# Kernel tuning notes

Hardware: AMD Instinct MI355X
Metric: run time of the kernel (lower is better)

Reference implementation:

```python
import jax, jax.numpy as jnp
import numpy as np

N_NODES = 50000
N_EDGES = 800000
N_GRAPHS = 64

def _glorot(key, shape, scale=0.05):
    return jax.random.normal(key, shape, dtype=jnp.float32) * scale

def setup_inputs() -> dict:
    key = jax.random.key(0)
    ks = jax.random.split(key, 32)
    inp = {
        'x': jax.random.normal(ks[0], (N_NODES, 17), dtype=jnp.float32),
        'edge_index': jax.random.randint(ks[1], (2, N_EDGES), 0, N_NODES, dtype=jnp.int64) if jax.config.jax_enable_x64 else jax.random.randint(ks[1], (2, N_EDGES), 0, N_NODES).astype(jnp.int32),
        'batch': jnp.sort(jax.random.randint(ks[2], (N_NODES,), 0, N_GRAPHS)),
        'observable_features': jax.random.normal(ks[3], (N_GRAPHS, 5), dtype=jnp.float32),
        'noise_factor': jax.random.uniform(ks[4], (N_GRAPHS, 1), dtype=jnp.float32),
        'noisy_exp': jax.random.normal(ks[5], (N_GRAPHS, 1), dtype=jnp.float32),
        # GATv2 layer 1: 17 -> 128 (heads=1)
        'Wl1': _glorot(ks[6], (17, 128)), 'bl1': jnp.zeros((128,), jnp.float32),
        'Wr1': _glorot(ks[7], (17, 128)), 'br1': jnp.zeros((128,), jnp.float32),
        'att1': _glorot(ks[8], (128,)), 'bias1': jnp.zeros((128,), jnp.float32),
        # GATv2 layer 2: 128 -> 32
        'Wl2': _glorot(ks[9], (128, 32)), 'bl2': jnp.zeros((32,), jnp.float32),
        'Wr2': _glorot(ks[10], (128, 32)), 'br2': jnp.zeros((32,), jnp.float32),
        'att2': _glorot(ks[11], (32,)), 'bias2': jnp.zeros((32,), jnp.float32),
        # obs_encoder: 5 -> 32 -> 8
        'Wo1': _glorot(ks[12], (5, 32)), 'bo1': jnp.zeros((32,), jnp.float32),
        'Wo2': _glorot(ks[13], (32, 8)), 'bo2': jnp.zeros((8,), jnp.float32),
        # noise_encoder: 1 -> 4
        'Wn': _glorot(ks[14], (1, 4)), 'bn': jnp.zeros((4,), jnp.float32),
        # fusion: 45 -> 256 -> 32 -> 1 (dropout inactive at eval)
        'Wf1': _glorot(ks[15], (45, 256)), 'bf1': jnp.zeros((256,), jnp.float32),
        'Wf2': _glorot(ks[16], (256, 32)), 'bf2': jnp.zeros((32,), jnp.float32),
        'Wf3': _glorot(ks[17], (32, 1)), 'bf3': jnp.zeros((1,), jnp.float32),
    }
    return inp

def gatv2_layer(x, src, dst, Wl, bl, Wr, br, att, bias, n_nodes):
    # PyG GATv2Conv, heads=1, concat=True, negative_slope=0.2
    xl = x @ Wl + bl            # source transform  [N, d]
    xr = x @ Wr + br            # target transform  [N, d]
    e = jax.nn.leaky_relu(xl[src] + xr[dst], 0.2)   # [E, d]
    score = e @ att                                   # [E]
    # softmax over incoming edges per target node (stable)
    m = jax.ops.segment_max(score, dst, num_segments=n_nodes)
    ex = jnp.exp(score - m[dst])
    denom = jax.ops.segment_sum(ex, dst, num_segments=n_nodes)
    alpha = ex / (denom[dst] + 1e-16)
    out = jax.ops.segment_sum(alpha[:, None] * xl[src], dst, num_segments=n_nodes)
    return out + bias

def _forward(x, edge_index, batch, observable_features, noise_factor, noisy_exp,
             Wl1, bl1, Wr1, br1, att1, bias1,
             Wl2, bl2, Wr2, br2, att2, bias2,
             Wo1, bo1, Wo2, bo2, Wn, bn,
             Wf1, bf1, Wf2, bf2, Wf3, bf3):
    n = x.shape[0]
    # add self loops (GATv2Conv default add_self_loops=True)
    loops = jnp.arange(n, dtype=edge_index.dtype)
    src = jnp.concatenate([edge_index[0], loops])
    dst = jnp.concatenate([edge_index[1], loops])
    h = jax.nn.elu(gatv2_layer(x, src, dst, Wl1, bl1, Wr1, br1, att1, bias1, n))
    h = jax.nn.elu(gatv2_layer(h, src, dst, Wl2, bl2, Wr2, br2, att2, bias2, n))
    # global mean pool over graphs
    sums = jax.ops.segment_sum(h, batch, num_segments=N_GRAPHS)
    cnts = jax.ops.segment_sum(jnp.ones((n,), h.dtype), batch, num_segments=N_GRAPHS)
    circuit_embedding = sums / jnp.maximum(cnts, 1.0)[:, None]     # [G, 32]
    obs_embedding = jax.nn.relu(observable_features @ Wo1 + bo1) @ Wo2 + bo2  # [G, 8]
    noise_embedding = noise_factor @ Wn + bn                        # [G, 4]
    combined = jnp.concatenate([circuit_embedding, obs_embedding, noise_embedding,
                                noisy_exp.reshape(-1, 1)], axis=1)  # [G, 45]
    hfc = jax.nn.relu(combined @ Wf1 + bf1)
    hfc = jax.nn.relu(hfc @ Wf2 + bf2)
    correction = hfc @ Wf3 + bf3                                    # [G, 1]
    return noisy_exp + correction

def reference(x, edge_index, batch, observable_features, noise_factor, noisy_exp,
              Wl1, bl1, Wr1, br1, att1, bias1,
              Wl2, bl2, Wr2, br2, att2, bias2,
              Wo1, bo1, Wo2, bo2, Wn, bn,
              Wf1, bf1, Wf2, bf2, Wf3, bf3):
    return _forward(x, edge_index, batch, observable_features, noise_factor, noisy_exp,
                    Wl1, bl1, Wr1, br1, att1, bias1,
                    Wl2, bl2, Wr2, br2, att2, bias2,
                    Wo1, bo1, Wo2, bo2, Wn, bn,
                    Wf1, bf1, Wf2, bf2, Wf3, bf3)
```

## Files before the change

kernel.cpp:

```cpp
#include <hip/hip_runtime.h>
#include <math.h>

#define DEV __device__ __forceinline__

typedef __attribute__((ext_vector_type(8))) short bf16x8;
typedef __attribute__((ext_vector_type(4))) float f32x4;
typedef __attribute__((ext_vector_type(2))) float f32x2;

#define CAP 64
#define HB 4
#define BCAP 1536
#define BCS 16

DEV f32x2 pk_add(f32x2 a, f32x2 b) {
    f32x2 d;
    asm("v_pk_add_f32 %0, %1, %2" : "=v"(d) : "v"(a), "v"(b));
    return d;
}
DEV f32x2 pk_fma(f32x2 a, f32x2 b, f32x2 c) {
    f32x2 d;
    asm("v_pk_fma_f32 %0, %1, %2, %3" : "=v"(d) : "v"(a), "v"(b), "v"(c));
    return d;
}

template<int CTRL>
DEV float dpp_add(float x) {
    int y = __builtin_amdgcn_update_dpp(0, __float_as_int(x), CTRL, 0xf, 0xf, true);
    return x + __int_as_float(y);
}
DEV float sum16(float p) {
    p = dpp_add<0x121>(p);
    p = dpp_add<0x122>(p);
    p = dpp_add<0x124>(p);
    p = dpp_add<0x128>(p);
    return p;
}

DEV unsigned short bf16r(float f) {
    unsigned u = __float_as_uint(f);
    return (unsigned short)((u + 0x7FFFu + ((u >> 16) & 1u)) >> 16);
}
DEV unsigned pack_bf16(float a, float b) {
    return (unsigned)bf16r(a) | ((unsigned)bf16r(b) << 16);
}
DEV f32x2 up2(unsigned u) {
    f32x2 v;
    v.x = __uint_as_float(u << 16);
    v.y = __uint_as_float(u & 0xFFFF0000u);
    return v;
}

__global__ void k_zero(int* __restrict__ bcnt, int NB16, float* __restrict__ pooled, int PN) {
    int i = blockIdx.x * blockDim.x + threadIdx.x;
    int s = gridDim.x * blockDim.x;
    for (int j = i; j < NB16; j += s) bcnt[j] = 0;
    for (int j = i; j < PN; j += s) pooled[j] = 0.f;
}

__global__ void k_scatter(const int* __restrict__ ei, int E, int ET,
                          int* __restrict__ bcnt, unsigned* __restrict__ bbuf) {
    int idx = blockIdx.x * blockDim.x + threadIdx.x;
    int stride = gridDim.x * blockDim.x;
    int s[HB], d[HB]; bool v[HB];
#pragma unroll
    for (int c = 0; c < HB; c++) {
        int e = idx + c * stride;
        v[c] = e < ET;
        int ee = v[c] ? e : 0;
        s[c] = (ee < E) ? ei[ee] : (ee - E);
        d[c] = (ee < E) ? ei[E + ee] : (ee - E);
    }
    int sl[HB];
#pragma unroll
    for (int c = 0; c < HB; c++)
        sl[c] = v[c] ? atomicAdd(bcnt + (d[c] >> 6) * BCS, 1) : BCAP;
#pragma unroll
    for (int c = 0; c < HB; c++)
        if (v[c] && sl[c] < BCAP)
            bbuf[(size_t)(d[c] >> 6) * BCAP + sl[c]] =
                (unsigned)s[c] | ((unsigned)d[c] << 16);
}

__global__ void __launch_bounds__(256) k_bucket(
        const int* __restrict__ bcnt, const unsigned* __restrict__ bbuf,
        unsigned short* __restrict__ seg, int* __restrict__ cnt, int N) {
    __shared__ int lcnt[64];
    int b = blockIdx.x;
    int t = threadIdx.x;
    if (t < 64) lcnt[t] = 0;
    __syncthreads();
    int bc = bcnt[b * BCS];
    if (bc > BCAP) bc = BCAP;
    int base = b << 6;
    const unsigned* bp = bbuf + (size_t)b * BCAP;
    for (int i = t; i < bc; i += 256) {
        unsigned ev = bp[i];
        int s = ev & 0xFFFF;
        int d = ev >> 16;
        int slot = atomicAdd(&lcnt[d - base], 1);
        if (slot < CAP) seg[(size_t)d * CAP + slot] = (unsigned short)s;
    }
    __syncthreads();
    if (t < 64 && base + t < N) cnt[base + t] = lcnt[t];
}

__global__ void __launch_bounds__(256) k_xform1(
        const float* __restrict__ x,
        const float* __restrict__ Wl, const float* __restrict__ bl,
        const float* __restrict__ Wr, const float* __restrict__ br,
        unsigned* __restrict__ xlb, unsigned* __restrict__ xrb, int N) {
    int lane = threadIdx.x & 63;
    int d0 = 2 * lane;
    float wl0[17], wl1[17], wr0[17], wr1[17];
#pragma unroll
    for (int k = 0; k < 17; k++) {
        wl0[k] = Wl[k * 128 + d0];
        wl1[k] = Wl[k * 128 + d0 + 1];
        wr0[k] = Wr[k * 128 + d0];
        wr1[k] = Wr[k * 128 + d0 + 1];
    }
    float bl0 = bl[d0], bl1v = bl[d0 + 1], br0 = br[d0], br1v = br[d0 + 1];
    int wid = (blockIdx.x * blockDim.x + threadIdx.x) >> 6;
    int nw = gridDim.x * (blockDim.x >> 6);
    for (int n0 = wid; n0 < N; n0 += nw) {
        int n = __builtin_amdgcn_readfirstlane(n0);
        const float* xp = x + (size_t)n * 17;
        float xk[17];
#pragma unroll
        for (int k = 0; k < 17; k++) xk[k] = xp[k];
        float a0 = bl0, a1 = bl1v, b0 = br0, b1 = br1v;
#pragma unroll
        for (int k = 0; k < 17; k++) {
            a0 = fmaf(xk[k], wl0[k], a0);
            a1 = fmaf(xk[k], wl1[k], a1);
            b0 = fmaf(xk[k], wr0[k], b0);
            b1 = fmaf(xk[k], wr1[k], b1);
        }
        xlb[(size_t)n * 64 + lane] = pack_bf16(a0, a1);
        xrb[(size_t)n * 64 + lane] = pack_bf16(b0, b1);
    }
}

#define CH1 4
__global__ void k_agg1(const int* __restrict__ cnt, const unsigned short* __restrict__ seg,
                       const uint4* __restrict__ xlb, const uint4* __restrict__ xrb,
                       const float* __restrict__ att, const float* __restrict__ bias,
                       uint4* __restrict__ h1b, int N) {
    int node = (blockIdx.x * blockDim.x + threadIdx.x) >> 4;
    int sub = threadIdx.x & 15;
    if (node >= N) return;
    int je = cnt[node];
    if (je > CAP) je = CAP;
    const unsigned short* rowu = seg + (size_t)node * CAP;
    f32x2 r2[4];
    {
        uint4 rv = xrb[node * 16 + sub];
        r2[0] = up2(rv.x); r2[1] = up2(rv.y); r2[2] = up2(rv.z); r2[3] = up2(rv.w);
    }
    const float4* att4 = (const float4*)att;
    float4 aa = att4[sub * 2], ab = att4[sub * 2 + 1];
    f32x2 a6[4], a4[4];
    a6[0].x = 0.6f * aa.x; a6[0].y = 0.6f * aa.y;
    a6[1].x = 0.6f * aa.z; a6[1].y = 0.6f * aa.w;
    a6[2].x = 0.6f * ab.x; a6[2].y = 0.6f * ab.y;
    a6[3].x = 0.6f * ab.z; a6[3].y = 0.6f * ab.w;
    a4[0].x = 0.4f * aa.x; a4[0].y = 0.4f * aa.y;
    a4[1].x = 0.4f * aa.z; a4[1].y = 0.4f * aa.w;
    a4[2].x = 0.4f * ab.x; a4[2].y = 0.4f * ab.y;
    a4[3].x = 0.4f * ab.z; a4[3].y = 0.4f * ab.w;
    f32x2 acc2[4];
#pragma unroll
    for (int j = 0; j < 4; j++) { acc2[j].x = 0.f; acc2[j].y = 0.f; }
    float den = 0.f;
    for (int j0 = 0; j0 < je; j0 += CH1) {
        uint2 sv = *(const uint2*)(rowu + j0);
        int s[CH1];
        s[0] = sv.x & 0xFFFF;
        s[1] = (j0 + 1 < je) ? (int)(sv.x >> 16) : s[0];
        s[2] = (j0 + 2 < je) ? (int)(sv.y & 0xFFFF) : s[0];
        s[3] = (j0 + 3 < je) ? (int)(sv.y >> 16) : s[0];
        uint4 lv[CH1];
        f32x2 l[CH1][4];
        float p[CH1];
#pragma unroll
        for (int c = 0; c < CH1; c++) lv[c] = xlb[s[c] * 16 + sub];
#pragma unroll
        for (int c = 0; c < CH1; c++) {
            l[c][0] = up2(lv[c].x); l[c][1] = up2(lv[c].y);
            l[c][2] = up2(lv[c].z); l[c][3] = up2(lv[c].w);
        }
#pragma unroll
        for (int c = 0; c < CH1; c++) {
            f32x2 q2; q2.x = 0.f; q2.y = 0.f;
#pragma unroll
            for (int j = 0; j < 4; j++) {
                f32x2 v = pk_add(l[c][j], r2[j]);
                f32x2 av;
                av.x = fabsf(v.x); av.y = fabsf(v.y);
                q2 = pk_fma(v, a6[j], q2);
                q2 = pk_fma(av, a4[j], q2);
            }
            p[c] = q2.x + q2.y;
        }
#pragma unroll
        for (int c = 0; c < CH1; c++) p[c] = sum16(p[c]);
#pragma unroll
        for (int c = 0; c < CH1; c++) {
            float e = (j0 + c < je) ? __expf(p[c]) : 0.f;
            den += e;
            f32x2 e2; e2.x = e; e2.y = e;
#pragma unroll
            for (int j = 0; j < 4; j++) acc2[j] = pk_fma(l[c][j], e2, acc2[j]);
        }
    }
    float inv = 1.f / (den + 1e-16f);
    const float4* bias4 = (const float4*)bias;
    float4 b0 = bias4[sub * 2], b1 = bias4[sub * 2 + 1];
    float o[8];
    o[0] = acc2[0].x * inv + b0.x; o[1] = acc2[0].y * inv + b0.y;
    o[2] = acc2[1].x * inv + b0.z; o[3] = acc2[1].y * inv + b0.w;
    o[4] = acc2[2].x * inv + b1.x; o[5] = acc2[2].y * inv + b1.y;
    o[6] = acc2[3].x * inv + b1.z; o[7] = acc2[3].y * inv + b1.w;
#pragma unroll
    for (int d = 0; d < 8; d++) o[d] = (o[d] > 0.f) ? o[d] : expm1f(o[d]);
    uint4 ov;
    ov.x = pack_bf16(o[0], o[1]); ov.y = pack_bf16(o[2], o[3]);
    ov.z = pack_bf16(o[4], o[5]); ov.w = pack_bf16(o[6], o[7]);
    h1b[node * 16 + sub] = ov;
}

__global__ void __launch_bounds__(256) k_xform2(
        const unsigned short* __restrict__ h1b,
        const float* __restrict__ Wl, const float* __restrict__ bl,
        const float* __restrict__ Wr, const float* __restrict__ br,
        unsigned short* __restrict__ xc2, int N) {
    int l = threadIdx.x & 63;
    int m = l & 15;
    int kg = l >> 4;
    bf16x8 w[4][4];
    float bias[4];
#pragma unroll
    for (int dt = 0; dt < 4; dt++) {
        int col = dt * 16 + m;
        const float* W = (col < 32) ? Wl : Wr;
        int c = col & 31;
        bias[dt] = (col < 32) ? bl[c] : br[c];
#pragma unroll
        for (int kc = 0; kc < 4; kc++) {
#pragma unroll
            for (int i = 0; i < 8; i++) {
                int k = kc * 32 + kg * 8 + i;
                w[dt][kc][i] = (short)bf16r(W[k * 32 + c]);
            }
        }
    }
    int ntiles = (N + 15) >> 4;
    int wid = (blockIdx.x * blockDim.x + threadIdx.x) >> 6;
    int nw = gridDim.x * (blockDim.x >> 6);
    for (int tb = wid; tb < ntiles; tb += nw) {
        int arow = tb * 16 + m;
        if (arow >= N) arow = N - 1;
        const bf16x8* ap = (const bf16x8*)(h1b + (size_t)arow * 128);
        f32x4 acc0 = {0.f, 0.f, 0.f, 0.f}, acc1 = acc0, acc2 = acc0, acc3 = acc0;
#pragma unroll
        for (int kc = 0; kc < 4; kc++) {
            bf16x8 a = ap[kc * 4 + kg];
            acc0 = __builtin_amdgcn_mfma_f32_16x16x32_bf16(a, w[0][kc], acc0, 0, 0, 0);
            acc1 = __builtin_amdgcn_mfma_f32_16x16x32_bf16(a, w[1][kc], acc1, 0, 0, 0);
            acc2 = __builtin_amdgcn_mfma_f32_16x16x32_bf16(a, w[2][kc], acc2, 0, 0, 0);
            acc3 = __builtin_amdgcn_mfma_f32_16x16x32_bf16(a, w[3][kc], acc3, 0, 0, 0);
        }
#pragma unroll
        for (int j = 0; j < 4; j++) {
            int orow = tb * 16 + kg * 4 + j;
            if (orow < N) {
                size_t base = (size_t)orow * 64 + m;
                xc2[base]      = bf16r(acc0[j] + bias[0]);
                xc2[base + 16] = bf16r(acc1[j] + bias[1]);
                xc2[base + 32] = bf16r(acc2[j] + bias[2]);
                xc2[base + 48] = bf16r(acc3[j] + bias[3]);
            }
        }
    }
}

#define CH2 8
__global__ void k_agg2(const int* __restrict__ cnt, const unsigned short* __restrict__ seg,
                       const unsigned* __restrict__ xc2,
                       const float* __restrict__ att, const float* __restrict__ bias,
                       float2* __restrict__ h2, int N) {
    int node = (blockIdx.x * blockDim.x + threadIdx.x) >> 4;
    int sub = threadIdx.x & 15;
    if (node >= N) return;
    int je = cnt[node];
    if (je > CAP) je = CAP;
    const unsigned short* rowu = seg + (size_t)node * CAP;
    f32x2 r2 = up2(xc2[node * 32 + 16 + sub]);
    float2 a = reinterpret_cast<const float2*>(att)[sub];
    f32x2 a6, a4;
    a6.x = 0.6f * a.x; a6.y = 0.6f * a.y;
    a4.x = 0.4f * a.x; a4.y = 0.4f * a.y;
    float den = 0.f;
    f32x2 acc; acc.x = 0.f; acc.y = 0.f;
    for (int j0 = 0; j0 < je; j0 += CH2) {
        uint4 sv = *(const uint4*)(rowu + j0);
        int s[CH2];
        s[0] = sv.x & 0xFFFF;
        s[1] = (j0 + 1 < je) ? (int)(sv.x >> 16) : s[0];
        s[2] = (j0 + 2 < je) ? (int)(sv.y & 0xFFFF) : s[0];
        s[3] = (j0 + 3 < je) ? (int)(sv.y >> 16) : s[0];
        s[4] = (j0 + 4 < je) ? (int)(sv.z & 0xFFFF) : s[0];
        s[5] = (j0 + 5 < je) ? (int)(sv.z >> 16) : s[0];
        s[6] = (j0 + 6 < je) ? (int)(sv.w & 0xFFFF) : s[0];
        s[7] = (j0 + 7 < je) ? (int)(sv.w >> 16) : s[0];
        f32x2 l[CH2];
        float p[CH2];
#pragma unroll
        for (int c = 0; c < CH2; c++) l[c] = up2(xc2[s[c] * 32 + sub]);
#pragma unroll
        for (int c = 0; c < CH2; c++) {
            f32x2 v = pk_add(l[c], r2);
            f32x2 av;
            av.x = fabsf(v.x); av.y = fabsf(v.y);
            f32x2 q2; q2.x = 0.f; q2.y = 0.f;
            q2 = pk_fma(v, a6, q2);
            q2 = pk_fma(av, a4, q2);
            p[c] = q2.x + q2.y;
        }
#pragma unroll
        for (int c = 0; c < CH2; c++) p[c] = sum16(p[c]);
#pragma unroll
        for (int c = 0; c < CH2; c++) {
            float e = (j0 + c < je) ? __expf(p[c]) : 0.f;
            den += e;
            f32x2 e2; e2.x = e; e2.y = e;
            acc = pk_fma(l[c], e2, acc);
        }
    }
    float inv = 1.f / (den + 1e-16f);
    float2 b = reinterpret_cast<const float2*>(bias)[sub];
    float2 o;
    o.x = acc.x * inv + b.x; o.x = (o.x > 0.f) ? o.x : expm1f(o.x);
    o.y = acc.y * inv + b.y; o.y = (o.y > 0.f) ? o.y : expm1f(o.y);
    h2[node * 16 + sub] = o;
}

__global__ void k_pool(const float* __restrict__ h2, const int* __restrict__ batch,
                       float* __restrict__ pooled, int N, int G) {
    int gid = (blockIdx.x * blockDim.x + threadIdx.x) >> 5;
    int d = threadIdx.x & 31;
    int r0 = gid * 8;
    if (r0 >= N) return;
    int rend = r0 + 8; if (rend > N) rend = N;
    int gcur = batch[r0];
    float acc = 0.f;
    for (int r = r0; r < rend; r++) {
        int g = batch[r];
        if (g != gcur) {
            atomicAdd(pooled + gcur * 32 + d, acc);
            acc = 0.f;
            gcur = g;
        }
        acc += h2[(size_t)r * 32 + d];
    }
    atomicAdd(pooled + gcur * 32 + d, acc);
}

__global__ void k_head(const float* __restrict__ pooled, const int* __restrict__ batch,
                       int N, int G,
                       const float* __restrict__ obs, const float* __restrict__ nf,
                       const float* __restrict__ ne,
                       const float* __restrict__ Wo1, const float* __restrict__ bo1,
                       const float* __restrict__ Wo2, const float* __restrict__ bo2,
                       const float* __restrict__ Wn, const float* __restrict__ bn,
                       const float* __restrict__ Wf1, const float* __restrict__ bf1,
                       const float* __restrict__ Wf2, const float* __restrict__ bf2,
                       const float* __restrict__ Wf3, const float* __restrict__ bf3,
                       float* __restrict__ out) {
    __shared__ float comb[45];
    __shared__ float ho[32];
    __shared__ float hh1[256];
    __shared__ float hh2[32];
    __shared__ int bounds[2];
    int g = blockIdx.x;
    int t = threadIdx.x;
    if (t < 2) {
        int target = g + t;
        if (target >= G) bounds[t] = N;
        else {
            int lo = 0, hi = N;
            while (lo < hi) {
                int mid = (lo + hi) >> 1;
                if (batch[mid] < target) lo = mid + 1; else hi = mid;
            }
            bounds[t] = lo;
        }
    }
    __syncthreads();
    int s0 = bounds[0], s1 = bounds[1];
    if (t < 32) {
        float c = (float)(s1 - s0);
        c = (c > 1.f) ? c : 1.f;
        comb[t] = pooled[g * 32 + t] / c;
        float a = bo1[t];
#pragma unroll
        for (int k = 0; k < 5; k++) a += obs[g * 5 + k] * Wo1[k * 32 + t];
        ho[t] = (a > 0.f) ? a : 0.f;
    }
    __syncthreads();
    if (t < 8) {
        float a = bo2[t];
#pragma unroll
        for (int k = 0; k < 32; k++) a += ho[k] * Wo2[k * 8 + t];
        comb[32 + t] = a;
    }
    if (t >= 8 && t < 12) {
        int dd = t - 8;
        comb[40 + dd] = nf[g] * Wn[dd] + bn[dd];
    }
    if (t == 12) comb[44] = ne[g];
    __syncthreads();
    {
        float a = bf1[t];
#pragma unroll
        for (int k = 0; k < 45; k++) a += comb[k] * Wf1[k * 256 + t];
        hh1[t] = (a > 0.f) ? a : 0.f;
    }
    __syncthreads();
    if (t < 32) {
        float a = bf2[t];
#pragma unroll
        for (int k = 0; k < 256; k++) a += hh1[k] * Wf2[k * 32 + t];
        hh2[t] = (a > 0.f) ? a : 0.f;
    }
    __syncthreads();
    if (t == 0) {
        float a = bf3[0];
#pragma unroll
        for (int k = 0; k < 32; k++) a += hh2[k] * Wf3[k];
        out[g] = ne[g] + a;
    }
}

extern "C" void kernel_launch(void* const* d_in, const int* in_sizes, int n_in,
                              void* d_out, int out_size, void* d_ws, size_t ws_size,
                              hipStream_t stream) {
    const float* x = (const float*)d_in[0];
    const int* ei = (const int*)d_in[1];
    const int* batch = (const int*)d_in[2];
    const float* obs = (const float*)d_in[3];
    const float* nf = (const float*)d_in[4];
    const float* ne = (const float*)d_in[5];
    const float* Wl1 = (const float*)d_in[6];
    const float* bl1 = (const float*)d_in[7];
    const float* Wr1 = (const float*)d_in[8];
    const float* br1 = (const float*)d_in[9];
    const float* att1 = (const float*)d_in[10];
    const float* bias1 = (const float*)d_in[11];
    const float* Wl2 = (const float*)d_in[12];
    const float* bl2 = (const float*)d_in[13];
    const float* Wr2 = (const float*)d_in[14];
    const float* br2 = (const float*)d_in[15];
    const float* att2 = (const float*)d_in[16];
    const float* bias2 = (const float*)d_in[17];
    const float* Wo1 = (const float*)d_in[18];
    const float* bo1 = (const float*)d_in[19];
    const float* Wo2 = (const float*)d_in[20];
    const float* bo2 = (const float*)d_in[21];
    const float* Wn = (const float*)d_in[22];
    const float* bn = (const float*)d_in[23];
    const float* Wf1 = (const float*)d_in[24];
    const float* bf1 = (const float*)d_in[25];
    const float* Wf2 = (const float*)d_in[26];
    const float* bf2 = (const float*)d_in[27];
    const float* Wf3 = (const float*)d_in[28];
    const float* bf3 = (const float*)d_in[29];

    const int N = in_sizes[0] / 17;
    const int E = in_sizes[1] / 2;
    const int G = in_sizes[3] / 5;
    const int ET = E + N;
    const int NBK = (N + 63) / 64;

    float* ws = (float*)d_ws;
    size_t o = 0;
    unsigned* xlb = (unsigned*)(ws + o); o += (size_t)N * 64;
    unsigned* xrb = (unsigned*)(ws + o); o += (size_t)N * 64;
    unsigned* h1b = (unsigned*)(ws + o); o += (size_t)N * 64;
    unsigned short* seg = (unsigned short*)(ws + o); o += (size_t)N * 32;
    int* cnt = (int*)(ws + o); o += (size_t)N;
    float* pooled = ws + o; o += (size_t)G * 32;
    int* bcnt = (int*)(ws + o); o += (size_t)NBK * BCS;
    unsigned* bbuf = (unsigned*)(ws + o); o += (size_t)NBK * BCAP;
    unsigned short* xc2 = (unsigned short*)xlb;
    float* h2 = (float*)xrb;

    const int eb4 = (ET + 256 * HB - 1) / (256 * HB);

    k_zero<<<64, 256, 0, stream>>>(bcnt, NBK * BCS, pooled, G * 32);
    k_scatter<<<eb4, 256, 0, stream>>>(ei, E, ET, bcnt, bbuf);
    k_bucket<<<NBK, 256, 0, stream>>>(bcnt, bbuf, seg, cnt, N);

    k_xform1<<<512, 256, 0, stream>>>(x, Wl1, bl1, Wr1, br1, xlb, xrb, N);
    k_agg1<<<(N * 16 + 255) / 256, 256, 0, stream>>>(cnt, seg, (const uint4*)xlb,
                                                     (const uint4*)xrb, att1, bias1,
                                                     (uint4*)h1b, N);

    k_xform2<<<160, 256, 0, stream>>>((const unsigned short*)h1b, Wl2, bl2, Wr2, br2,
                                      xc2, N);
    k_agg2<<<(N * 16 + 255) / 256, 256, 0, stream>>>(cnt, seg, (const unsigned*)xc2,
                                                     att2, bias2, (float2*)h2, N);

    {
        int ngroups = (N + 7) / 8;
        int nthreads = ngroups * 32;
        k_pool<<<(nthreads + 255) / 256, 256, 0, stream>>>(h2, batch, pooled, N, G);
    }
    k_head<<<G, 256, 0, stream>>>(pooled, batch, N, G, obs, nf, ne,
                                  Wo1, bo1, Wo2, bo2, Wn, bn,
                                  Wf1, bf1, Wf2, bf2, Wf3, bf3,
                                  (float*)d_out);
}
```

Measured before the change: 178.4 us.

## Fuse edge CSR fill with layer-1 transform and fold pooling into agg2

Replaces the two-pass bucketed scatter (global bucket buffer plus per-bucket LDS sort) with direct per-node global atomics into the segment array. That fill now runs in the same launch as the layer-1 feature transform, split by block index. Mean-pool accumulation moves into the layer-2 aggregation epilogue via per-node atomics, which drops the h2 buffer and the separate pool kernel. This saves launches and memory round trips, but adds heavy global atomic contention on pooled (64 graphs by 32 floats) and scattered atomics on cnt.

```diff
diff --git a/kernel.cpp b/kernel.cpp
--- a/kernel.cpp
+++ b/kernel.cpp
@@ -9,8 +9,6 @@
 
 #define CAP 64
 #define HB 4
-#define BCAP 1536
-#define BCS 16
 
 DEV f32x2 pk_add(f32x2 a, f32x2 b) {
     f32x2 d;
@@ -50,65 +48,41 @@
     return v;
 }
 
-__global__ void k_zero(int* __restrict__ bcnt, int NB16, float* __restrict__ pooled, int PN) {
+__global__ void k_zero(int* __restrict__ cnt, int N, float* __restrict__ pooled, int PN) {
     int i = blockIdx.x * blockDim.x + threadIdx.x;
     int s = gridDim.x * blockDim.x;
-    for (int j = i; j < NB16; j += s) bcnt[j] = 0;
+    for (int j = i; j < N; j += s) cnt[j] = 0;
     for (int j = i; j < PN; j += s) pooled[j] = 0.f;
 }
 
-__global__ void k_scatter(const int* __restrict__ ei, int E, int ET,
-                          int* __restrict__ bcnt, unsigned* __restrict__ bbuf) {
-    int idx = blockIdx.x * blockDim.x + threadIdx.x;
-    int stride = gridDim.x * blockDim.x;
-    int s[HB], d[HB]; bool v[HB];
-#pragma unroll
-    for (int c = 0; c < HB; c++) {
-        int e = idx + c * stride;
-        v[c] = e < ET;
-        int ee = v[c] ? e : 0;
-        s[c] = (ee < E) ? ei[ee] : (ee - E);
-        d[c] = (ee < E) ? ei[E + ee] : (ee - E);
-    }
-    int sl[HB];
-#pragma unroll
-    for (int c = 0; c < HB; c++)
-        sl[c] = v[c] ? atomicAdd(bcnt + (d[c] >> 6) * BCS, 1) : BCAP;
-#pragma unroll
-    for (int c = 0; c < HB; c++)
-        if (v[c] && sl[c] < BCAP)
-            bbuf[(size_t)(d[c] >> 6) * BCAP + sl[c]] =
-                (unsigned)s[c] | ((unsigned)d[c] << 16);
-}
-
-__global__ void __launch_bounds__(256) k_bucket(
-        const int* __restrict__ bcnt, const unsigned* __restrict__ bbuf,
-        unsigned short* __restrict__ seg, int* __restrict__ cnt, int N) {
-    __shared__ int lcnt[64];
-    int b = blockIdx.x;
-    int t = threadIdx.x;
-    if (t < 64) lcnt[t] = 0;
-    __syncthreads();
-    int bc = bcnt[b * BCS];
-    if (bc > BCAP) bc = BCAP;
-    int base = b << 6;
-    const unsigned* bp = bbuf + (size_t)b * BCAP;
-    for (int i = t; i < bc; i += 256) {
-        unsigned ev = bp[i];
-        int s = ev & 0xFFFF;
-        int d = ev >> 16;
-        int slot = atomicAdd(&lcnt[d - base], 1);
-        if (slot < CAP) seg[(size_t)d * CAP + slot] = (unsigned short)s;
-    }
-    __syncthreads();
-    if (t < 64 && base + t < N) cnt[base + t] = lcnt[t];
-}
-
-__global__ void __launch_bounds__(256) k_xform1(
+__global__ void __launch_bounds__(256) k_fillx1(
+        const int* __restrict__ ei, int E, int ET,
+        int* __restrict__ cnt, unsigned short* __restrict__ seg,
         const float* __restrict__ x,
         const float* __restrict__ Wl, const float* __restrict__ bl,
         const float* __restrict__ Wr, const float* __restrict__ br,
-        unsigned* __restrict__ xlb, unsigned* __restrict__ xrb, int N) {
+        unsigned* __restrict__ xlb, unsigned* __restrict__ xrb, int N, int FB) {
+    if (blockIdx.x < FB) {
+        int idx = blockIdx.x * blockDim.x + threadIdx.x;
+        int stride = FB * blockDim.x;
+        int s[HB], d[HB]; bool v[HB];
+#pragma unroll
+        for (int c = 0; c < HB; c++) {
+            int e = idx + c * stride;
+            v[c] = e < ET;
+            int ee = v[c] ? e : 0;
+            s[c] = (ee < E) ? ei[ee] : (ee - E);
+            d[c] = (ee < E) ? ei[E + ee] : (ee - E);
+        }
+        int sl[HB];
+#pragma unroll
+        for (int c = 0; c < HB; c++)
+            sl[c] = v[c] ? atomicAdd(cnt + d[c], 1) : CAP;
+#pragma unroll
+        for (int c = 0; c < HB; c++)
+            if (v[c] && sl[c] < CAP) seg[(size_t)d[c] * CAP + sl[c]] = (unsigned short)s[c];
+        return;
+    }
     int lane = threadIdx.x & 63;
     int d0 = 2 * lane;
     float wl0[17], wl1[17], wr0[17], wr1[17];
@@ -120,8 +94,10 @@
         wr1[k] = Wr[k * 128 + d0 + 1];
     }
     float bl0 = bl[d0], bl1v = bl[d0 + 1], br0 = br[d0], br1v = br[d0 + 1];
-    int wid = (blockIdx.x * blockDim.x + threadIdx.x) >> 6;
-    int nw = gridDim.x * (blockDim.x >> 6);
+    int xb = blockIdx.x - FB;
+    int nxb = gridDim.x - FB;
+    int wid = (xb * blockDim.x + threadIdx.x) >> 6;
+    int nw = nxb * (blockDim.x >> 6);
     for (int n0 = wid; n0 < N; n0 += nw) {
         int n = __builtin_amdgcn_readfirstlane(n0);
         const float* xp = x + (size_t)n * 17;
@@ -286,9 +262,9 @@
 
 #define CH2 8
 __global__ void k_agg2(const int* __restrict__ cnt, const unsigned short* __restrict__ seg,
-                       const unsigned* __restrict__ xc2,
+                       const unsigned* __restrict__ xc2, const int* __restrict__ batch,
                        const float* __restrict__ att, const float* __restrict__ bias,
-                       float2* __restrict__ h2, int N) {
+                       float* __restrict__ pooled, int N) {
     int node = (blockIdx.x * blockDim.x + threadIdx.x) >> 4;
     int sub = threadIdx.x & 15;
     if (node >= N) return;
@@ -339,31 +315,11 @@
     }
     float inv = 1.f / (den + 1e-16f);
     float2 b = reinterpret_cast<const float2*>(bias)[sub];
-    float2 o;
-    o.x = acc.x * inv + b.x; o.x = (o.x > 0.f) ? o.x : expm1f(o.x);
-    o.y = acc.y * inv + b.y; o.y = (o.y > 0.f) ? o.y : expm1f(o.y);
-    h2[node * 16 + sub] = o;
-}
-
-__global__ void k_pool(const float* __restrict__ h2, const int* __restrict__ batch,
-                       float* __restrict__ pooled, int N, int G) {
-    int gid = (blockIdx.x * blockDim.x + threadIdx.x) >> 5;
-    int d = threadIdx.x & 31;
-    int r0 = gid * 8;
-    if (r0 >= N) return;
-    int rend = r0 + 8; if (rend > N) rend = N;
-    int gcur = batch[r0];
-    float acc = 0.f;
-    for (int r = r0; r < rend; r++) {
-        int g = batch[r];
-        if (g != gcur) {
-            atomicAdd(pooled + gcur * 32 + d, acc);
-            acc = 0.f;
-            gcur = g;
-        }
-        acc += h2[(size_t)r * 32 + d];
-    }
-    atomicAdd(pooled + gcur * 32 + d, acc);
+    float ox = acc.x * inv + b.x; ox = (ox > 0.f) ? ox : expm1f(ox);
+    float oy = acc.y * inv + b.y; oy = (oy > 0.f) ? oy : expm1f(oy);
+    int g = batch[node];
+    atomicAdd(pooled + g * 32 + 2 * sub, ox);
+    atomicAdd(pooled + g * 32 + 2 * sub + 1, oy);
 }
 
 __global__ void k_head(const float* __restrict__ pooled, const int* __restrict__ batch,
@@ -480,7 +436,6 @@
     const int E = in_sizes[1] / 2;
     const int G = in_sizes[3] / 5;
     const int ET = E + N;
-    const int NBK = (N + 63) / 64;
 
     float* ws = (float*)d_ws;
     size_t o = 0;
@@ -490,18 +445,15 @@
     unsigned short* seg = (unsigned short*)(ws + o); o += (size_t)N * 32;
     int* cnt = (int*)(ws + o); o += (size_t)N;
     float* pooled = ws + o; o += (size_t)G * 32;
-    int* bcnt = (int*)(ws + o); o += (size_t)NBK * BCS;
-    unsigned* bbuf = (unsigned*)(ws + o); o += (size_t)NBK * BCAP;
     unsigned short* xc2 = (unsigned short*)xlb;
-    float* h2 = (float*)xrb;
-
-    const int eb4 = (ET + 256 * HB - 1) / (256 * HB);
-
-    k_zero<<<64, 256, 0, stream>>>(bcnt, NBK * BCS, pooled, G * 32);
-    k_scatter<<<eb4, 256, 0, stream>>>(ei, E, ET, bcnt, bbuf);
-    k_bucket<<<NBK, 256, 0, stream>>>(bcnt, bbuf, seg, cnt, N);
-
-    k_xform1<<<512, 256, 0, stream>>>(x, Wl1, bl1, Wr1, br1, xlb, xrb, N);
+
+    const int FB = (ET + 256 * HB - 1) / (256 * HB);
+    const int XB = 512;
+
+    k_zero<<<128, 256, 0, stream>>>(cnt, N, pooled, G * 32);
+    k_fillx1<<<FB + XB, 256, 0, stream>>>(ei, E, ET, cnt, seg,
+                                          x, Wl1, bl1, Wr1, br1, xlb, xrb, N, FB);
+
     k_agg1<<<(N * 16 + 255) / 256, 256, 0, stream>>>(cnt, seg, (const uint4*)xlb,
                                                      (const uint4*)xrb, att1, bias1,
                                                      (uint4*)h1b, N);
@@ -509,13 +461,8 @@
     k_xform2<<<160, 256, 0, stream>>>((const unsigned short*)h1b, Wl2, bl2, Wr2, br2,
                                       xc2, N);
     k_agg2<<<(N * 16 + 255) / 256, 256, 0, stream>>>(cnt, seg, (const unsigned*)xc2,
-                                                     att2, bias2, (float2*)h2, N);
-
-    {
-        int ngroups = (N + 7) / 8;
-        int nthreads = ngroups * 32;
-        k_pool<<<(nthreads + 255) / 256, 256, 0, stream>>>(h2, batch, pooled, N, G);
-    }
+                                                     batch, att2, bias2, pooled, N);
+
     k_head<<<G, 256, 0, stream>>>(pooled, batch, N, G, obs, nf, ne,
                                   Wo1, bo1, Wo2, bo2, Wn, bn,
                                   Wf1, bf1, Wf2, bf2, Wf3, bf3,
```

Measured after the change: 277.4 us. 1.55x slower.
